# Optimization experiments

Hardware: AMD Instinct MI355X
Metric: run time of the kernel (lower is better)

## Reference

```python
import jax, jax.numpy as jnp
import numpy as np

DEPTH = 9            # tree depth -> 2**DEPTH-1 = 511 nodes, 255 internal
ENSEMBLE = 16
CLASS_NUM = 10
IN_DIM = 784
HID = 128            # encode_feature_dimension for arch='mlp'
BATCH = 8192
INTERNAL = 2 ** (DEPTH - 1) - 1   # 255
TOTAL = 2 ** DEPTH - 1            # 511


def setup_inputs() -> dict:
    key = jax.random.key(0)
    ks = jax.random.split(key, 7)
    X = jax.random.normal(ks[0], (BATCH, IN_DIM), dtype=jnp.float32)
    W1 = jax.random.normal(ks[1], (IN_DIM, HID), dtype=jnp.float32) * 0.02
    b1 = jnp.zeros((HID,), jnp.float32)
    W2 = jax.random.normal(ks[2], (HID, CLASS_NUM), dtype=jnp.float32) * 0.02
    b2 = jnp.zeros((CLASS_NUM,), jnp.float32)
    # xavier-uniform style node weights: Linear(HID, 1) per internal node per tree
    limit = float(np.sqrt(6.0 / (HID + 1)))
    nodeW = jax.random.uniform(ks[3], (ENSEMBLE, INTERNAL, HID), jnp.float32, -limit, limit)
    nodeb = jnp.zeros((ENSEMBLE, INTERNAL), jnp.float32)
    return {"X": X, "W1": W1, "b1": b1, "W2": W2, "b2": b2, "nodeW": nodeW, "nodeb": nodeb}


def _tree_paths(feats, nodeW, nodeb):
    # feats: [B, HID]; nodeW: [T, I, HID]; nodeb: [T, I]
    # decisions for ALL internal nodes in one batched GEMM
    dec = jax.nn.sigmoid(jnp.einsum('bd,tid->tib', feats, nodeW) + nodeb[:, :, None])  # [T, I, B]
    T, I, B = dec.shape
    results = jnp.ones((T, TOTAL, B), feats.dtype)
    # level-wise parallel prefix product down the tree (loop over DEPTH-1 levels only)
    for lvl in range(DEPTH - 1):
        start = 2 ** lvl - 1
        cnt = 2 ** lvl
        parent = results[:, start:start + cnt]          # [T, cnt, B]
        d = dec[:, start:start + cnt]                   # [T, cnt, B]
        # children of parent i are 2i+1 (left: *d) and 2i+2 (right: *(1-d)),
        # contiguous + interleaved starting at 2*start+1 = 2**(lvl+1)-1
        children = jnp.stack([parent * d, parent * (1.0 - d)], axis=2).reshape(T, 2 * cnt, B)
        results = results.at[:, 2 * start + 1: 2 * start + 1 + 2 * cnt].set(children)
    return results  # [T, TOTAL, B]


def reference(X, W1, b1, W2, b2, nodeW, nodeb):
    feats = jax.nn.relu(X @ W1 + b1)          # encoder embedding [B, HID]
    prediction = feats @ W2 + b2              # auxiliary predictor [B, CLASS_NUM]
    all_results = _tree_paths(feats, nodeW, nodeb)  # [T, 2**D-1, B]
    return prediction, all_results
```

## Files before the change

### kernel.cpp

```cpp
#include <hip/hip_runtime.h>
#include <hip/hip_bf16.h>

#define BATCH 8192
#define IN_DIM 784
#define HID 128
#define CLS 10
#define ENSEMBLE 16
#define INTERNAL 255
#define TOTAL 511
#define KPAD 800

typedef __attribute__((ext_vector_type(8))) short short8;
typedef __attribute__((ext_vector_type(4))) float floatx4;


__device__ inline short f2bf(float f) {
  __hip_bfloat16 h = __float2bfloat16(f);
  return *reinterpret_cast<short*>(&h);
}

__global__ void convert_kernel(const float* __restrict__ W1,
                               const float* __restrict__ nodeW,
                               __hip_bfloat16* __restrict__ W1T,
                               __hip_bfloat16* __restrict__ nWbf) {
  const int N2 = HID * KPAD;
  const int N3 = ENSEMBLE * 256 * HID;
  const int total = N2 + N3;
  for (int i = blockIdx.x * blockDim.x + threadIdx.x; i < total;
       i += gridDim.x * blockDim.x) {
    if (i < N2) {
      int c = i / KPAD, k = i - c * KPAD;
      float v = (k < IN_DIM) ? W1[k * HID + c] : 0.0f;
      W1T[i] = __float2bfloat16(v);
    } else {
      int j = i - N2;
      int t = j >> 15;
      int r = j & 32767;
      int ii = r >> 7;
      int d = r & 127;
      float v = (ii < INTERNAL) ? nodeW[(t * INTERNAL + ii) * HID + d] : 0.0f;
      nWbf[j] = __float2bfloat16(v);
    }
  }
}

__global__ __launch_bounds__(256) void feats_kernel(
    const float* __restrict__ X,
    const __hip_bfloat16* __restrict__ W1T,
    const float* __restrict__ b1,
    __hip_bfloat16* __restrict__ featsbf) {
  const int wave = threadIdx.x >> 6;
  const int lane = threadIdx.x & 63;
  const int lo = lane & 15;
  const int q = lane >> 4;
  const int m0 = blockIdx.x * 16;
  const int cb = wave * 32;

  floatx4 acc0 = {0.f, 0.f, 0.f, 0.f};
  floatx4 acc1 = {0.f, 0.f, 0.f, 0.f};
  const short* Wp = (const short*)W1T;
  const float* Xrow = X + (size_t)(m0 + lo) * IN_DIM;

  for (int ks = 0; ks < KPAD / 32; ks++) {
    const int k0 = ks * 32 + q * 8;
    short8 a;
    if (k0 + 8 <= IN_DIM) {
      float4 x0 = *(const float4*)(Xrow + k0);
      float4 x1 = *(const float4*)(Xrow + k0 + 4);
      a[0] = f2bf(x0.x); a[1] = f2bf(x0.y); a[2] = f2bf(x0.z); a[3] = f2bf(x0.w);
      a[4] = f2bf(x1.x); a[5] = f2bf(x1.y); a[6] = f2bf(x1.z); a[7] = f2bf(x1.w);
    } else {
      a = (short8){0, 0, 0, 0, 0, 0, 0, 0};
    }
    short8 b0f = *(const short8*)(Wp + (size_t)(cb + lo) * KPAD + k0);
    short8 b1f = *(const short8*)(Wp + (size_t)(cb + 16 + lo) * KPAD + k0);
    acc0 = __builtin_amdgcn_mfma_f32_16x16x32_bf16(a, b0f, acc0, 0, 0, 0);
    acc1 = __builtin_amdgcn_mfma_f32_16x16x32_bf16(a, b1f, acc1, 0, 0, 0);
  }
#pragma unroll
  for (int nt = 0; nt < 2; nt++) {
    const floatx4 acc = nt ? acc1 : acc0;
    const int c = cb + nt * 16 + lo;
    const float bias = b1[c];
#pragma unroll
    for (int r = 0; r < 4; r++) {
      const int row = m0 + q * 4 + r;
      float v = fmaxf(acc[r] + bias, 0.0f);
      featsbf[(size_t)row * HID + c] = __float2bfloat16(v);
    }
  }
}

__global__ __launch_bounds__(256) void pred_kernel(
    const __hip_bfloat16* __restrict__ featsbf,
    const float* __restrict__ W2,
    const float* __restrict__ b2,
    float* __restrict__ out) {
  __shared__ float W2s[HID * CLS];
  __shared__ float b2s[CLS];
  for (int i = threadIdx.x; i < HID * CLS; i += 256) W2s[i] = W2[i];
  if (threadIdx.x < CLS) b2s[threadIdx.x] = b2[threadIdx.x];
  __syncthreads();
  int gid = blockIdx.x * 256 + threadIdx.x;
  if (gid >= BATCH * CLS) return;
  int b = gid / CLS, c = gid - b * CLS;
  const short* fr = (const short*)featsbf + (size_t)b * HID;
  float acc = b2s[c];
#pragma unroll
  for (int kk = 0; kk < HID / 8; kk++) {
    short8 f8 = *(const short8*)(fr + kk * 8);
#pragma unroll
    for (int j = 0; j < 8; j++) {
      unsigned u = ((unsigned)(unsigned short)f8[j]) << 16;
      acc += __uint_as_float(u) * W2s[(kk * 8 + j) * CLS + c];
    }
  }
  out[gid] = acc;
}

__global__ __launch_bounds__(256) void tree_kernel(
    const __hip_bfloat16* __restrict__ featsbf,
    const __hip_bfloat16* __restrict__ nWbf,
    const float* __restrict__ nodeb,
    float* __restrict__ out ) {
  __shared__ float dec_s[INTERNAL * 32];

  const int t = blockIdx.y;
  const int b0 = blockIdx.x * 32;
  const int tid = threadIdx.x;
  const int wave = tid >> 6;
  const int lane = tid & 63;
  const int lo = lane & 15;
  const int q = lane >> 4;

  const short* Fp = (const short*)featsbf;
  const short* Np = (const short*)nWbf;

  short8 bfr[2][4];
#pragma unroll
  for (int nt = 0; nt < 2; nt++)
#pragma unroll
    for (int ks = 0; ks < 4; ks++)
      bfr[nt][ks] =
          *(const short8*)(Fp + (size_t)(b0 + nt * 16 + lo) * HID + ks * 32 + q * 8);

#pragma unroll
  for (int mt = 0; mt < 4; mt++) {
    const int ibase = wave * 64 + mt * 16;
    floatx4 acc0 = {0.f, 0.f, 0.f, 0.f};
    floatx4 acc1 = {0.f, 0.f, 0.f, 0.f};
#pragma unroll
    for (int ks = 0; ks < 4; ks++) {
      short8 a = *(const short8*)(Np + (size_t)(t * 256 + ibase + lo) * HID +
                                  ks * 32 + q * 8);
      acc0 = __builtin_amdgcn_mfma_f32_16x16x32_bf16(a, bfr[0][ks], acc0, 0, 0, 0);
      acc1 = __builtin_amdgcn_mfma_f32_16x16x32_bf16(a, bfr[1][ks], acc1, 0, 0, 0);
    }
#pragma unroll
    for (int r = 0; r < 4; r++) {
      const int iloc = ibase + q * 4 + r;
      if (iloc < INTERNAL) {
        const float nb = nodeb[t * INTERNAL + iloc];
        dec_s[iloc * 32 + lo]      = 1.0f / (1.0f + __expf(-(acc0[r] + nb)));
        dec_s[iloc * 32 + 16 + lo] = 1.0f / (1.0f + __expf(-(acc1[r] + nb)));
      }
    }
  }
  __syncthreads();

  const int s = tid >> 5;
  const int b = tid & 31;
  float* outT = out + (size_t)t * TOTAL * BATCH + b0 + b;

  const float d0 = dec_s[0 * 32 + b];
  const float p1 = (s & 4) ? (1.0f - d0) : d0;
  const float d1 = dec_s[(1 + (s >> 2)) * 32 + b];
  const float p2 = p1 * ((s & 2) ? (1.0f - d1) : d1);
  const float d2 = dec_s[(3 + (s >> 1)) * 32 + b];
  const float p3 = p2 * ((s & 1) ? (1.0f - d2) : d2);

  if (s == 0) __builtin_nontemporal_store(1.0f, outT);
  if ((s & 3) == 0)
    __builtin_nontemporal_store(p1, outT + (size_t)(1 + (s >> 2)) * BATCH);
  if ((s & 1) == 0)
    __builtin_nontemporal_store(p2, outT + (size_t)(3 + (s >> 1)) * BATCH);
  __builtin_nontemporal_store(p3, outT + (size_t)(7 + s) * BATCH);

  float P[32];
  P[0] = p3;
#pragma unroll
  for (int r = 1; r <= 5; r++) {
    const int W = 1 << r;
    float nP[32];
#pragma unroll
    for (int i = 0; i < 32; i++) {
      if (i < W) {
        const int jp = (s << (r - 1)) + (i >> 1);
        const int ph = ((1 << (2 + r)) - 1) + jp;
        const float d = dec_s[ph * 32 + b];
        const float v = P[i >> 1] * ((i & 1) ? (1.0f - d) : d);
        nP[i] = v;
        const int ch = ((1 << (3 + r)) - 1) + (s << r) + i;
        __builtin_nontemporal_store(v, outT + (size_t)ch * BATCH);
      }
    }
#pragma unroll
    for (int i = 0; i < 32; i++)
      if (i < W) P[i] = nP[i];
  }
}

extern "C" void kernel_launch(void* const* d_in, const int* in_sizes, int n_in,
                              void* d_out, int out_size, void* d_ws, size_t ws_size,
                              hipStream_t stream) {
  const float* X = (const float*)d_in[0];
  const float* W1 = (const float*)d_in[1];
  const float* b1 = (const float*)d_in[2];
  const float* W2 = (const float*)d_in[3];
  const float* b2 = (const float*)d_in[4];
  const float* nodeW = (const float*)d_in[5];
  const float* nodeb = (const float*)d_in[6];

  float* pred_out = (float*)d_out;
  float* results_out = pred_out + BATCH * CLS;

  char* ws = (char*)d_ws;
  __hip_bfloat16* W1T = (__hip_bfloat16*)(ws + 0);
  __hip_bfloat16* nWbf = (__hip_bfloat16*)(ws + 204800);
  __hip_bfloat16* featsbf = (__hip_bfloat16*)(ws + 1253376);

  convert_kernel<<<612, 256, 0, stream>>>(W1, nodeW, W1T, nWbf);
  feats_kernel<<<BATCH / 16, 256, 0, stream>>>(X, W1T, b1, featsbf);
  pred_kernel<<<(BATCH * CLS + 255) / 256, 256, 0, stream>>>(featsbf, W2, b2, pred_out);
  tree_kernel<<<dim3(BATCH / 32, ENSEMBLE), 256, 0, stream>>>(featsbf, nWbf, nodeb,
                                                              results_out);
}
```

Before: 343.6 us.

## Fuse predictor into feats kernel and widen tree tiles with vector stores

The auxiliary predictor is computed inside the feature kernel from fp32 features staged in shared memory, which removes a separate launch and the bf16 reload. The tree kernel now handles 64 batch columns per block and keeps decisions in fp16 shared memory. Each thread writes four consecutive batch entries per node with 16-byte nontemporal stores instead of scalar stores. Storing decisions in fp16 adds rounding error to the path products, and the wider tile raises register pressure.

```diff
diff --git a/kernel.cpp b/kernel.cpp
--- a/kernel.cpp
+++ b/kernel.cpp
@@ -12,6 +12,7 @@
 
 typedef __attribute__((ext_vector_type(8))) short short8;
 typedef __attribute__((ext_vector_type(4))) float floatx4;
+typedef __attribute__((ext_vector_type(4))) _Float16 half4;
 
 
 __device__ inline short f2bf(float f) {
@@ -48,9 +49,20 @@
     const float* __restrict__ X,
     const __hip_bfloat16* __restrict__ W1T,
     const float* __restrict__ b1,
-    __hip_bfloat16* __restrict__ featsbf) {
-  const int wave = threadIdx.x >> 6;
-  const int lane = threadIdx.x & 63;
+    const float* __restrict__ W2,
+    const float* __restrict__ b2,
+    __hip_bfloat16* __restrict__ featsbf,
+    float* __restrict__ pred_out) {
+  __shared__ float feats_s[16 * HID];
+  __shared__ float W2s[HID * CLS];
+  __shared__ float b2s[CLS];
+
+  const int tid = threadIdx.x;
+  for (int i = tid; i < HID * CLS; i += 256) W2s[i] = W2[i];
+  if (tid < CLS) b2s[tid] = b2[tid];
+
+  const int wave = tid >> 6;
+  const int lane = tid & 63;
   const int lo = lane & 15;
   const int q = lane >> 4;
   const int m0 = blockIdx.x * 16;
@@ -84,38 +96,22 @@
     const float bias = b1[c];
 #pragma unroll
     for (int r = 0; r < 4; r++) {
-      const int row = m0 + q * 4 + r;
+      const int rl = q * 4 + r;
       float v = fmaxf(acc[r] + bias, 0.0f);
-      featsbf[(size_t)row * HID + c] = __float2bfloat16(v);
-    }
-  }
-}
-
-__global__ __launch_bounds__(256) void pred_kernel(
-    const __hip_bfloat16* __restrict__ featsbf,
-    const float* __restrict__ W2,
-    const float* __restrict__ b2,
-    float* __restrict__ out) {
-  __shared__ float W2s[HID * CLS];
-  __shared__ float b2s[CLS];
-  for (int i = threadIdx.x; i < HID * CLS; i += 256) W2s[i] = W2[i];
-  if (threadIdx.x < CLS) b2s[threadIdx.x] = b2[threadIdx.x];
+      featsbf[(size_t)(m0 + rl) * HID + c] = __float2bfloat16(v);
+      feats_s[rl * HID + c] = v;
+    }
+  }
   __syncthreads();
-  int gid = blockIdx.x * 256 + threadIdx.x;
-  if (gid >= BATCH * CLS) return;
-  int b = gid / CLS, c = gid - b * CLS;
-  const short* fr = (const short*)featsbf + (size_t)b * HID;
-  float acc = b2s[c];
-#pragma unroll
-  for (int kk = 0; kk < HID / 8; kk++) {
-    short8 f8 = *(const short8*)(fr + kk * 8);
-#pragma unroll
-    for (int j = 0; j < 8; j++) {
-      unsigned u = ((unsigned)(unsigned short)f8[j]) << 16;
-      acc += __uint_as_float(u) * W2s[(kk * 8 + j) * CLS + c];
-    }
-  }
-  out[gid] = acc;
+
+  if (tid < 16 * CLS) {
+    const int r = tid / CLS, c = tid - r * CLS;
+    float acc = b2s[c];
+    const float* fr = feats_s + r * HID;
+#pragma unroll 8
+    for (int k = 0; k < HID; k++) acc += fr[k] * W2s[k * CLS + c];
+    pred_out[(size_t)(m0 + r) * CLS + c] = acc;
+  }
 }
 
 __global__ __launch_bounds__(256) void tree_kernel(
@@ -123,10 +119,10 @@
     const __hip_bfloat16* __restrict__ nWbf,
     const float* __restrict__ nodeb,
     float* __restrict__ out ) {
-  __shared__ float dec_s[INTERNAL * 32];
+  __shared__ _Float16 dec_s[INTERNAL * 64];
 
   const int t = blockIdx.y;
-  const int b0 = blockIdx.x * 32;
+  const int b0 = blockIdx.x * 64;
   const int tid = threadIdx.x;
   const int wave = tid >> 6;
   const int lane = tid & 63;
@@ -136,9 +132,9 @@
   const short* Fp = (const short*)featsbf;
   const short* Np = (const short*)nWbf;
 
-  short8 bfr[2][4];
-#pragma unroll
-  for (int nt = 0; nt < 2; nt++)
+  short8 bfr[4][4];
+#pragma unroll
+  for (int nt = 0; nt < 4; nt++)
 #pragma unroll
     for (int ks = 0; ks < 4; ks++)
       bfr[nt][ks] =
@@ -147,67 +143,104 @@
 #pragma unroll
   for (int mt = 0; mt < 4; mt++) {
     const int ibase = wave * 64 + mt * 16;
-    floatx4 acc0 = {0.f, 0.f, 0.f, 0.f};
-    floatx4 acc1 = {0.f, 0.f, 0.f, 0.f};
+    floatx4 acc[4];
+#pragma unroll
+    for (int nt = 0; nt < 4; nt++) acc[nt] = (floatx4){0.f, 0.f, 0.f, 0.f};
 #pragma unroll
     for (int ks = 0; ks < 4; ks++) {
       short8 a = *(const short8*)(Np + (size_t)(t * 256 + ibase + lo) * HID +
                                   ks * 32 + q * 8);
-      acc0 = __builtin_amdgcn_mfma_f32_16x16x32_bf16(a, bfr[0][ks], acc0, 0, 0, 0);
-      acc1 = __builtin_amdgcn_mfma_f32_16x16x32_bf16(a, bfr[1][ks], acc1, 0, 0, 0);
+#pragma unroll
+      for (int nt = 0; nt < 4; nt++)
+        acc[nt] = __builtin_amdgcn_mfma_f32_16x16x32_bf16(a, bfr[nt][ks], acc[nt], 0, 0, 0);
     }
 #pragma unroll
     for (int r = 0; r < 4; r++) {
       const int iloc = ibase + q * 4 + r;
       if (iloc < INTERNAL) {
         const float nb = nodeb[t * INTERNAL + iloc];
-        dec_s[iloc * 32 + lo]      = 1.0f / (1.0f + __expf(-(acc0[r] + nb)));
-        dec_s[iloc * 32 + 16 + lo] = 1.0f / (1.0f + __expf(-(acc1[r] + nb)));
+#pragma unroll
+        for (int nt = 0; nt < 4; nt++) {
+          const float sig = 1.0f / (1.0f + __expf(-(acc[nt][r] + nb)));
+          dec_s[iloc * 64 + nt * 16 + lo] = (_Float16)sig;
+        }
       }
     }
   }
   __syncthreads();
 
-  const int s = tid >> 5;
-  const int b = tid & 31;
-  float* outT = out + (size_t)t * TOTAL * BATCH + b0 + b;
-
-  const float d0 = dec_s[0 * 32 + b];
-  const float p1 = (s & 4) ? (1.0f - d0) : d0;
-  const float d1 = dec_s[(1 + (s >> 2)) * 32 + b];
-  const float p2 = p1 * ((s & 2) ? (1.0f - d1) : d1);
-  const float d2 = dec_s[(3 + (s >> 1)) * 32 + b];
-  const float p3 = p2 * ((s & 1) ? (1.0f - d2) : d2);
-
-  if (s == 0) __builtin_nontemporal_store(1.0f, outT);
-  if ((s & 3) == 0)
-    __builtin_nontemporal_store(p1, outT + (size_t)(1 + (s >> 2)) * BATCH);
-  if ((s & 1) == 0)
-    __builtin_nontemporal_store(p2, outT + (size_t)(3 + (s >> 1)) * BATCH);
-  __builtin_nontemporal_store(p3, outT + (size_t)(7 + s) * BATCH);
-
-  float P[32];
-  P[0] = p3;
-#pragma unroll
-  for (int r = 1; r <= 5; r++) {
-    const int W = 1 << r;
-    float nP[32];
-#pragma unroll
-    for (int i = 0; i < 32; i++) {
-      if (i < W) {
-        const int jp = (s << (r - 1)) + (i >> 1);
-        const int ph = ((1 << (2 + r)) - 1) + jp;
-        const float d = dec_s[ph * 32 + b];
-        const float v = P[i >> 1] * ((i & 1) ? (1.0f - d) : d);
-        nP[i] = v;
-        const int ch = ((1 << (3 + r)) - 1) + (s << r) + i;
-        __builtin_nontemporal_store(v, outT + (size_t)ch * BATCH);
-      }
-    }
-#pragma unroll
-    for (int i = 0; i < 32; i++)
-      if (i < W) P[i] = nP[i];
-  }
+  const int s4 = tid >> 4;
+  const int bq = tid & 15;
+  float* outT = out + (size_t)t * TOTAL * BATCH + b0 + bq * 4;
+
+#define LOAD4(node)                                              \
+  ({                                                             \
+    half4 _h = *(const half4*)(dec_s + (node) * 64 + bq * 4);    \
+    (floatx4){(float)_h[0], (float)_h[1], (float)_h[2], (float)_h[3]}; \
+  })
+#define NTS(node, v) \
+  __builtin_nontemporal_store((v), (floatx4*)(outT + (size_t)(node) * BATCH))
+
+  floatx4 d, p;
+  d = LOAD4(0);
+  p = (s4 & 8) ? (1.0f - d) : d;
+  if (s4 == 0) NTS(0, ((floatx4){1.f, 1.f, 1.f, 1.f}));
+  if ((s4 & 7) == 0) NTS(1 + (s4 >> 3), p);
+  d = LOAD4(1 + (s4 >> 3));
+  p = p * ((s4 & 4) ? (1.0f - d) : d);
+  if ((s4 & 3) == 0) NTS(3 + (s4 >> 2), p);
+  d = LOAD4(3 + (s4 >> 2));
+  p = p * ((s4 & 2) ? (1.0f - d) : d);
+  if ((s4 & 1) == 0) NTS(7 + (s4 >> 1), p);
+  d = LOAD4(7 + (s4 >> 1));
+  p = p * ((s4 & 1) ? (1.0f - d) : d);
+  NTS(15 + s4, p);
+
+  floatx4 P[8];
+  P[0] = p;
+  {
+    floatx4 dv = LOAD4(15 + s4);
+    floatx4 c0 = P[0] * dv, c1 = P[0] * (1.0f - dv);
+    NTS(31 + 2 * s4 + 0, c0);
+    NTS(31 + 2 * s4 + 1, c1);
+    P[0] = c0; P[1] = c1;
+  }
+  {
+    floatx4 C[4];
+#pragma unroll
+    for (int ip = 0; ip < 2; ip++) {
+      floatx4 dv = LOAD4(31 + 2 * s4 + ip);
+      C[2 * ip] = P[ip] * dv;
+      C[2 * ip + 1] = P[ip] * (1.0f - dv);
+      NTS(63 + 4 * s4 + 2 * ip + 0, C[2 * ip]);
+      NTS(63 + 4 * s4 + 2 * ip + 1, C[2 * ip + 1]);
+    }
+#pragma unroll
+    for (int i = 0; i < 4; i++) P[i] = C[i];
+  }
+  {
+    floatx4 C[8];
+#pragma unroll
+    for (int ip = 0; ip < 4; ip++) {
+      floatx4 dv = LOAD4(63 + 4 * s4 + ip);
+      C[2 * ip] = P[ip] * dv;
+      C[2 * ip + 1] = P[ip] * (1.0f - dv);
+      NTS(127 + 8 * s4 + 2 * ip + 0, C[2 * ip]);
+      NTS(127 + 8 * s4 + 2 * ip + 1, C[2 * ip + 1]);
+    }
+#pragma unroll
+    for (int i = 0; i < 8; i++) P[i] = C[i];
+  }
+  {
+#pragma unroll
+    for (int ip = 0; ip < 8; ip++) {
+      floatx4 dv = LOAD4(127 + 8 * s4 + ip);
+      NTS(255 + 16 * s4 + 2 * ip + 0, P[ip] * dv);
+      NTS(255 + 16 * s4 + 2 * ip + 1, P[ip] * (1.0f - dv));
+    }
+  }
+#undef LOAD4
+#undef NTS
 }
 
 extern "C" void kernel_launch(void* const* d_in, const int* in_sizes, int n_in,
@@ -230,8 +263,7 @@
   __hip_bfloat16* featsbf = (__hip_bfloat16*)(ws + 1253376);
 
   convert_kernel<<<612, 256, 0, stream>>>(W1, nodeW, W1T, nWbf);
-  feats_kernel<<<BATCH / 16, 256, 0, stream>>>(X, W1T, b1, featsbf);
-  pred_kernel<<<(BATCH * CLS + 255) / 256, 256, 0, stream>>>(featsbf, W2, b2, pred_out);
-  tree_kernel<<<dim3(BATCH / 32, ENSEMBLE), 256, 0, stream>>>(featsbf, nWbf, nodeb,
+  feats_kernel<<<BATCH / 16, 256, 0, stream>>>(X, W1T, b1, W2, b2, featsbf, pred_out);
+  tree_kernel<<<dim3(BATCH / 64, ENSEMBLE), 256, 0, stream>>>(featsbf, nWbf, nodeb,
                                                               results_out);
 }
```

After: 334.8 us. -2.6%, faster.
